# Kernel tuning notes

Hardware: AMD Instinct MI355X
Metric: run time of the kernel (lower is better)

## Reference

```python
import jax, jax.numpy as jnp
import numpy as np

B, S, D = 64, 256, 512          # batch, seq_len_max, num_dim (= in_dim = nclass)
H, DO = 8, 64                   # num_heads, out_dim per head (H*DO == D)
ALPHA = 0.2                     # leaky_relu negative slope
N = B * S                       # nodes
DEG = 32
E = N * DEG + N                 # random edges + self-loops


def setup_inputs() -> dict:
    key = jax.random.key(0)
    k = jax.random.split(key, 7)
    h = jax.random.normal(k[0], (B, S, D), jnp.float32)
    loops = jnp.arange(N, dtype=jnp.int32)
    src = jnp.concatenate([jax.random.randint(k[1], (N * DEG,), 0, N, jnp.int32), loops])
    dst = jnp.concatenate([jax.random.randint(k[2], (N * DEG,), 0, N, jnp.int32), loops])
    W1 = jax.random.normal(k[3], (H, D, DO), jnp.float32) * 0.05      # per-head fc weight
    a1 = jax.random.normal(k[4], (H, 2 * DO), jnp.float32) * 0.05     # per-head attn_fc weight
    Wout = jax.random.normal(k[5], (H * DO, D), jnp.float32) * 0.05   # out_att fc
    aout = jax.random.normal(k[6], (2 * D,), jnp.float32) * 0.05      # out_att attn_fc
    return {"h": h, "W1": W1, "a1": a1, "Wout": Wout, "aout": aout, "src": src, "dst": dst}


def gat_head(x, W, a, src, dst, concat):
    # x: [N, in_d], W: [in_d, d], a: [2d]
    z = x @ W                                   # [N, d]
    d = W.shape[1]
    es = z @ a[:d]                              # src part of attn score, [N]
    ed = z @ a[d:]                              # dst part, [N]
    e = jax.nn.leaky_relu(es[src] + ed[dst], ALPHA)   # [E]
    # segment softmax over incoming edges of each dst node
    m = jax.ops.segment_max(e, dst, num_segments=N)
    m = jnp.where(jnp.isfinite(m), m, 0.0)
    ex = jnp.exp(e - m[dst])
    den = jax.ops.segment_sum(ex, dst, num_segments=N)
    att = ex / den[dst]                         # [E] (self-loops guarantee den > 0)
    out = jax.ops.segment_sum(att[:, None] * z[src], dst, num_segments=N)  # [N, d]
    return jax.nn.elu(out) if concat else out


def reference(h, W1, a1, Wout, aout, src, dst):
    x = h.reshape(N, D)                         # dropout is identity at eval
    heads = jax.vmap(lambda W, a: gat_head(x, W, a, src, dst, True))(W1, a1)  # [H, N, DO]
    hcat = jnp.transpose(heads, (1, 0, 2)).reshape(N, H * DO)                 # [N, H*DO]
    out = jax.nn.elu(gat_head(hcat, Wout, aout, src, dst, False))             # [N, D]
    return (out + x).reshape(B, S, D)
```

## Files before the change

### kernel.cpp

```cpp
#include <hip/hip_runtime.h>
#include <stdint.h>

#define DD 512
#define HH 8
#define DOO 64
#define ALPHA 0.2f

typedef __attribute__((ext_vector_type(8))) short short8;
typedef __attribute__((ext_vector_type(4))) float floatx4;
typedef __attribute__((ext_vector_type(4))) unsigned short u16x4;
typedef unsigned short u16;

static __device__ __forceinline__ float bf2f(u16 u){
  union { unsigned int u; float f; } c; c.u = ((unsigned int)u) << 16; return c.f;
}
static __device__ __forceinline__ u16 f2bf(float f){
  union { float f; unsigned int u; } c; c.f = f;
  unsigned int u = c.u;
  unsigned int r = (u + 0x7FFFu + ((u >> 16) & 1u)) >> 16;
  return (u16)r;
}
static __device__ __forceinline__ float leaky(float s){ return (s >= 0.f) ? s : ALPHA * s; }
static __device__ __forceinline__ float elu(float v){ return (v > 0.f) ? v : (__expf(v) - 1.f); }

#define PERM_LO 0x01000504u
#define PERM_HI 0x03020706u

#define DOT2(accv, pairv, wv) \
  asm("v_dot2_f32_bf16 %0, %1, %2, %0" : "+v"(accv) : "v"(pairv), "v"(wv))

#define DOTS8(ZA, ZB, AQ) do{ unsigned pr_; \
  pr_=__builtin_amdgcn_perm((ZA).x,(ZB).x,PERM_LO); DOT2(acc[0],pr_,(AQ)); \
  pr_=__builtin_amdgcn_perm((ZA).x,(ZB).x,PERM_HI); DOT2(acc[1],pr_,(AQ)); \
  pr_=__builtin_amdgcn_perm((ZA).y,(ZB).y,PERM_LO); DOT2(acc[2],pr_,(AQ)); \
  pr_=__builtin_amdgcn_perm((ZA).y,(ZB).y,PERM_HI); DOT2(acc[3],pr_,(AQ)); \
  pr_=__builtin_amdgcn_perm((ZA).z,(ZB).z,PERM_LO); DOT2(acc[4],pr_,(AQ)); \
  pr_=__builtin_amdgcn_perm((ZA).z,(ZB).z,PERM_HI); DOT2(acc[5],pr_,(AQ)); \
  pr_=__builtin_amdgcn_perm((ZA).w,(ZB).w,PERM_LO); DOT2(acc[6],pr_,(AQ)); \
  pr_=__builtin_amdgcn_perm((ZA).w,(ZB).w,PERM_HI); DOT2(acc[7],pr_,(AQ)); \
}while(0)

#define GLOAD_LDS16(g, l) \
  __builtin_amdgcn_global_load_lds((const __attribute__((address_space(1))) void*)(g), \
                                   (__attribute__((address_space(3))) void*)(l), 16, 0, 0)

static __device__ __forceinline__ uint4 rowl(const u16* __restrict__ zp, int s, int lane){
  return ((const uint4*)(zp + ((size_t)(unsigned)s << 9)))[lane];
}

__global__ void k_prep(const float* __restrict__ h, u16* __restrict__ xb,
                       const float* __restrict__ W1, u16* __restrict__ wbt1,
                       const float* __restrict__ Wout, u16* __restrict__ wbt2,
                       const int* __restrict__ dst, int* deg,
                       int n4, int E){
  int i = blockIdx.x * blockDim.x + threadIdx.x;
  if (i < n4){
    float4 v = ((const float4*)h)[i];
    u16x4 o;
    o[0] = f2bf(v.x); o[1] = f2bf(v.y); o[2] = f2bf(v.z); o[3] = f2bf(v.w);
    ((u16x4*)xb)[i] = o;
    return;
  }
  i -= n4;
  if (i < HH * DD * DOO / 8){
    int idx0 = i * 8;
    #pragma unroll
    for (int t = 0; t < 8; t++){
      int idx = idx0 + t;
      int hh = idx >> 15;
      int rem = idx & 32767;
      int k = rem >> 6;
      int dd = rem & 63;
      wbt1[(hh * 64 + dd) * DD + k] = f2bf(W1[idx]);
    }
    return;
  }
  i -= HH * DD * DOO / 8;
  if (i < DD * DD){
    int k = i >> 9, n = i & 511;
    wbt2[n * DD + k] = f2bf(Wout[i]);
    return;
  }
  i -= DD * DD;
  if (i < E) atomicAdd(&deg[dst[i]], 1);
}

__global__ void k_scan(const int* __restrict__ deg, int* __restrict__ off, int N){
  __shared__ int sm[1024];
  int tid = threadIdx.x;
  const int per = 16;
  int base = tid * per;
  int loc[per];
  int t = 0;
  #pragma unroll
  for (int i = 0; i < per; i++){
    int v = (base + i < N) ? deg[base + i] : 0;
    v = (v + 3) & ~3;
    loc[i] = v; t += v;
  }
  sm[tid] = t; __syncthreads();
  for (int o = 1; o < 1024; o <<= 1){
    int v = 0;
    if (tid >= o) v = sm[tid - o];
    __syncthreads();
    sm[tid] += v;
    __syncthreads();
  }
  int run = sm[tid] - t;
  #pragma unroll
  for (int i = 0; i < per; i++){ if (base + i < N) off[base + i] = run; run += loc[i]; }
  if (tid == 1023) off[N] = run;
}

__global__ void k_scatter(const int* __restrict__ src, const int* __restrict__ dst,
                          const int* __restrict__ off, int* cursor, int* __restrict__ csr,
                          int E, int N){
  int i = blockIdx.x * blockDim.x + threadIdx.x;
  if (i < 256){
    csr[off[N] + i] = 0;
  }
  if (i < E){
    int d = dst[i];
    int p = atomicAdd(&cursor[d], 1);
    csr[off[d] + p] = src[i];
  }
}

__global__ __launch_bounds__(256) void k_gemm(const u16* __restrict__ A,
                                              const u16* __restrict__ BT,
                                              u16* __restrict__ C, int M){
  __shared__ __attribute__((aligned(16))) u16 As[128 * 64];
  __shared__ __attribute__((aligned(16))) u16 Bs[128 * 64];
  const int tid = threadIdx.x;
  const int wid = tid >> 6, lane = tid & 63;
  const int n0 = blockIdx.x * 128, m0 = blockIdx.y * 128;
  const int wr = wid >> 1, wc = wid & 1;
  const int row16 = lane & 15, kg = lane >> 4;
  floatx4 acc[4][4];
  #pragma unroll
  for (int i = 0; i < 4; i++)
    #pragma unroll
    for (int j = 0; j < 4; j++) acc[i][j] = (floatx4)0.0f;

  for (int kt = 0; kt < DD; kt += 64){
    #pragma unroll
    for (int i = 0; i < 4; i++){
      int chunk = i * 256 + tid;
      int m = chunk >> 3, g = chunk & 7;
      int gs = g ^ (m & 7);
      GLOAD_LDS16(A + (size_t)(m0 + m) * DD + kt + gs * 8, &As[chunk * 8]);
      GLOAD_LDS16(BT + (size_t)(n0 + m) * DD + kt + gs * 8, &Bs[chunk * 8]);
    }
    __syncthreads();
    short8 af[4][2], bf[4][2];
    #pragma unroll
    for (int mi = 0; mi < 4; mi++)
      #pragma unroll
      for (int kk = 0; kk < 2; kk++){
        int row = wr * 64 + mi * 16 + row16;
        int gr = (kk * 4 + kg) ^ (row & 7);
        af[mi][kk] = *(const short8*)(&As[(row * 8 + gr) * 8]);
      }
    #pragma unroll
    for (int ni = 0; ni < 4; ni++)
      #pragma unroll
      for (int kk = 0; kk < 2; kk++){
        int row = wc * 64 + ni * 16 + row16;
        int gr = (kk * 4 + kg) ^ (row & 7);
        bf[ni][kk] = *(const short8*)(&Bs[(row * 8 + gr) * 8]);
      }
    #pragma unroll
    for (int kk = 0; kk < 2; kk++)
      #pragma unroll
      for (int mi = 0; mi < 4; mi++)
        #pragma unroll
        for (int ni = 0; ni < 4; ni++)
          acc[mi][ni] = __builtin_amdgcn_mfma_f32_16x16x32_bf16(af[mi][kk], bf[ni][kk], acc[mi][ni], 0, 0, 0);
    __syncthreads();
  }
  #pragma unroll
  for (int mi = 0; mi < 4; mi++)
    #pragma unroll
    for (int ni = 0; ni < 4; ni++)
      #pragma unroll
      for (int j = 0; j < 4; j++){
        int r = m0 + wr * 64 + mi * 16 + kg * 4 + j;
        int c = n0 + wc * 64 + ni * 16 + row16;
        C[(size_t)r * DD + c] = f2bf(acc[mi][ni][j]);
      }
}

__global__ void k_scores1(const u16* __restrict__ z, const float* __restrict__ a1,
                          float* __restrict__ es, float* __restrict__ ed, int N){
  int wid = threadIdx.x >> 6, lane = threadIdx.x & 63;
  int n = blockIdx.x * 4 + wid;
  if (n >= N) return;
  int h = lane >> 3, j8 = lane & 7;
  short8 zv = *(const short8*)(z + (size_t)n * DD + lane * 8);
  float esv = 0.f, edv = 0.f;
  #pragma unroll
  for (int t = 0; t < 8; t++){
    float f = bf2f((u16)zv[t]);
    esv += f * a1[h * 128 + j8 * 8 + t];
    edv += f * a1[h * 128 + 64 + j8 * 8 + t];
  }
  #pragma unroll
  for (int d2 = 1; d2 < 8; d2 <<= 1){ esv += __shfl_xor(esv, d2); edv += __shfl_xor(edv, d2); }
  if (j8 == 0){ es[n * 8 + h] = esv; ed[n * 8 + h] = edv; }
}

__global__ void k_scores2(const u16* __restrict__ z, const float* __restrict__ aout,
                          float* __restrict__ es, float* __restrict__ ed, int N){
  int wid = threadIdx.x >> 6, lane = threadIdx.x & 63;
  int n = blockIdx.x * 4 + wid;
  if (n >= N) return;
  short8 zv = *(const short8*)(z + (size_t)n * DD + lane * 8);
  float esv = 0.f, edv = 0.f;
  #pragma unroll
  for (int t = 0; t < 8; t++){
    float f = bf2f((u16)zv[t]);
    esv += f * aout[lane * 8 + t];
    edv += f * aout[512 + lane * 8 + t];
  }
  #pragma unroll
  for (int d2 = 1; d2 < 64; d2 <<= 1){ esv += __shfl_xor(esv, d2); edv += __shfl_xor(edv, d2); }
  if (lane == 0){ es[n] = esv; ed[n] = edv; }
}

__global__ void k_edgew1(const float* __restrict__ es, const float* __restrict__ ed,
                         const int* __restrict__ off, const int* __restrict__ deg,
                         int* __restrict__ csr, unsigned* __restrict__ wp,
                         float* __restrict__ den1, int N){
  int wid = threadIdx.x >> 6, lane = threadIdx.x & 63;
  int n = blockIdx.x * 4 + wid;
  if (n >= N) return;
  int o0 = off[n], cntp = off[n + 1] - o0, cnt = deg[n];
  float edh[8];
  {
    float4 d0 = *(const float4*)(ed + (size_t)n * 8);
    float4 d1 = *(const float4*)(ed + (size_t)n * 8 + 4);
    edh[0]=d0.x; edh[1]=d0.y; edh[2]=d0.z; edh[3]=d0.w;
    edh[4]=d1.x; edh[5]=d1.y; edh[6]=d1.z; edh[7]=d1.w;
  }
  float den[8];
  #pragma unroll
  for (int h = 0; h < 8; h++) den[h] = 0.f;
  for (int base = 0; base < cntp; base += 64){
    int e = base + lane;
    float wv[8];
    if (e < cnt){
      int s = csr[o0 + e];
      float4 e0 = *(const float4*)(es + (size_t)s * 8);
      float4 e1 = *(const float4*)(es + (size_t)s * 8 + 4);
      float ev[8] = {e0.x, e0.y, e0.z, e0.w, e1.x, e1.y, e1.z, e1.w};
      #pragma unroll
      for (int h = 0; h < 8; h++){
        float w = __expf(leaky(ev[h] + edh[h]));
        wv[h] = w; den[h] += w;
      }
    } else {
      if (e < cntp) csr[o0 + e] = 0;
      #pragma unroll
      for (int h = 0; h < 8; h++) wv[h] = 0.f;
    }
    unsigned pk[8];
    #pragma unroll
    for (int h = 0; h < 8; h++){
      float wn = __shfl_down(wv[h], 1);
      asm("v_cvt_pk_bf16_f32 %0, %1, %2" : "=v"(pk[h]) : "v"(wv[h]), "v"(wn));
    }
    if (!(lane & 1) && e < cntp){
      size_t q = (size_t)((o0 + e) >> 1) * 8;
      uint4 v0; v0.x = pk[0]; v0.y = pk[1]; v0.z = pk[2]; v0.w = pk[3];
      uint4 v1; v1.x = pk[4]; v1.y = pk[5]; v1.z = pk[6]; v1.w = pk[7];
      *(uint4*)(wp + q) = v0;
      *(uint4*)(wp + q + 4) = v1;
    }
  }
  #pragma unroll
  for (int h = 0; h < 8; h++){
    float d = den[h];
    #pragma unroll
    for (int d2 = 1; d2 < 64; d2 <<= 1) d += __shfl_xor(d, d2);
    if (lane == 0) den1[(size_t)n * 8 + h] = d;
  }
}

__global__ void k_edgew2(const float* __restrict__ es, const float* __restrict__ ed,
                         const int* __restrict__ off, const int* __restrict__ deg,
                         int* __restrict__ csr, unsigned* __restrict__ wp,
                         float* __restrict__ den2, int N){
  int wid = threadIdx.x >> 6, lane = threadIdx.x & 63;
  int n = blockIdx.x * 4 + wid;
  if (n >= N) return;
  int o0 = off[n], cntp = off[n + 1] - o0, cnt = deg[n];
  float edn = ed[n];
  float dsum = 0.f;
  for (int base = 0; base < cntp; base += 64){
    int e = base + lane;
    float w = 0.f;
    if (e < cnt){
      int s = csr[o0 + e];
      w = __expf(leaky(es[s] + edn));
      dsum += w;
    } else if (e < cntp){
      csr[o0 + e] = 0;
    }
    float wn = __shfl_down(w, 1);
    if (!(lane & 1) && e < cntp){
      unsigned pk;
      asm("v_cvt_pk_bf16_f32 %0, %1, %2" : "=v"(pk) : "v"(w), "v"(wn));
      wp[(o0 + e) >> 1] = pk;
    }
  }
  #pragma unroll
  for (int d2 = 1; d2 < 64; d2 <<= 1) dsum += __shfl_xor(dsum, d2);
  if (lane == 0) den2[n] = dsum;
}

__global__ __launch_bounds__(256) void k_agg1(const u16* __restrict__ z,
    const unsigned* __restrict__ wp, const float* __restrict__ den1,
    const int* __restrict__ off, const int* __restrict__ csr,
    u16* __restrict__ hcat, int N){
  int wid = __builtin_amdgcn_readfirstlane(threadIdx.x >> 6);
  int lane = threadIdx.x & 63;
  int n = blockIdx.x * 4 + wid;
  if (n >= N) return;
  int o0 = off[n];
  int itn = (off[n + 1] - o0) >> 2;
  const int4* cp4 = (const int4*)(csr + o0);
  int pb = o0 >> 1;
  int head = lane >> 3;
  const unsigned* wpb = wp + (size_t)pb * 8 + head;
  float acc[8];
  #pragma unroll
  for (int j = 0; j < 8; j++) acc[j] = 0.f;

  uint4 zA0, zA1, zB0, zB1;
  unsigned aqA, aqB;
  int4 c1;
  {
    int4 c0 = cp4[0];
    c1 = cp4[1];
    zA0 = rowl(z, c0.x, lane); zA1 = rowl(z, c0.y, lane);
    zB0 = rowl(z, c0.z, lane); zB1 = rowl(z, c0.w, lane);
    aqA = wpb[0]; aqB = wpb[8];
  }
  for (int it = 0; it < itn; ++it){
    int4 cn = cp4[it + 2];
    uint4 nA0 = rowl(z, c1.x, lane), nA1 = rowl(z, c1.y, lane);
    uint4 nB0 = rowl(z, c1.z, lane), nB1 = rowl(z, c1.w, lane);
    unsigned naqA = wpb[(size_t)(2 * it + 2) * 8];
    unsigned naqB = wpb[(size_t)(2 * it + 3) * 8];
    DOTS8(zA0, zA1, aqA);
    DOTS8(zB0, zB1, aqB);
    zA0 = nA0; zA1 = nA1; zB0 = nB0; zB1 = nB1;
    aqA = naqA; aqB = naqB; c1 = cn;
  }
  float inv = 1.f / den1[(size_t)n * 8 + head];
  short8 o;
  #pragma unroll
  for (int j = 0; j < 8; j++) o[j] = (short)f2bf(elu(acc[j] * inv));
  *(short8*)(hcat + (size_t)n * DD + lane * 8) = o;
}

__global__ __launch_bounds__(256) void k_agg2(const u16* __restrict__ z,
    const unsigned* __restrict__ wp, const float* __restrict__ den2,
    const int* __restrict__ off, const int* __restrict__ csr,
    const u16* __restrict__ xb, float* __restrict__ out, int N){
  int wid = __builtin_amdgcn_readfirstlane(threadIdx.x >> 6);
  int lane = threadIdx.x & 63;
  int n = blockIdx.x * 4 + wid;
  if (n >= N) return;
  int o0 = off[n];
  int itn = (off[n + 1] - o0) >> 2;
  const int4* cp4 = (const int4*)(csr + o0);
  int pb = o0 >> 1;
  float acc[8];
  #pragma unroll
  for (int j = 0; j < 8; j++) acc[j] = 0.f;

  uint4 zA0, zA1, zB0, zB1;
  unsigned aqA, aqB;
  int4 c1;
  {
    int4 c0 = cp4[0];
    c1 = cp4[1];
    zA0 = rowl(z, c0.x, lane); zA1 = rowl(z, c0.y, lane);
    zB0 = rowl(z, c0.z, lane); zB1 = rowl(z, c0.w, lane);
    uint2 a01 = *(const uint2*)(wp + pb);
    aqA = a01.x; aqB = a01.y;
  }
  for (int it = 0; it < itn; ++it){
    int4 cn = cp4[it + 2];
    uint4 nA0 = rowl(z, c1.x, lane), nA1 = rowl(z, c1.y, lane);
    uint4 nB0 = rowl(z, c1.z, lane), nB1 = rowl(z, c1.w, lane);
    uint2 an = *(const uint2*)(wp + pb + 2 * it + 2);
    DOTS8(zA0, zA1, aqA);
    DOTS8(zB0, zB1, aqB);
    zA0 = nA0; zA1 = nA1; zB0 = nB0; zB1 = nB1;
    aqA = an.x; aqB = an.y; c1 = cn;
  }
  float inv = 1.f / den2[n];
  short8 xv = *(const short8*)(xb + (size_t)n * DD + lane * 8);
  float ov[8];
  #pragma unroll
  for (int j = 0; j < 8; j++) ov[j] = elu(acc[j] * inv) + bf2f((u16)xv[j]);
  float4 o0v, o1v;
  o0v.x = ov[0]; o0v.y = ov[1]; o0v.z = ov[2]; o0v.w = ov[3];
  o1v.x = ov[4]; o1v.y = ov[5]; o1v.z = ov[6]; o1v.w = ov[7];
  *(float4*)(out + (size_t)n * DD + lane * 8) = o0v;
  *(float4*)(out + (size_t)n * DD + lane * 8 + 4) = o1v;
}

extern "C" void kernel_launch(void* const* d_in, const int* in_sizes, int n_in,
                              void* d_out, int out_size, void* d_ws, size_t ws_size,
                              hipStream_t stream){
  const float* h   = (const float*)d_in[0];
  const float* W1  = (const float*)d_in[1];
  const float* a1  = (const float*)d_in[2];
  const float* Wout= (const float*)d_in[3];
  const float* aout= (const float*)d_in[4];
  const int* src   = (const int*)d_in[5];
  const int* dst   = (const int*)d_in[6];
  float* out = (float*)d_out;
  const int N = in_sizes[0] / DD;
  const int E = in_sizes[5];
  const int EP = E + 3 * N + 512;
  const int ep2 = EP >> 1;

  char* p = (char*)d_ws;
  auto alloc = [&](size_t bytes) -> char* {
    char* r = p;
    p += (bytes + 255) & ~(size_t)255;
    return r;
  };
  u16* xb    = (u16*)alloc((size_t)N * DD * 2);
  u16* z1b   = (u16*)alloc((size_t)N * DD * 2);
  u16* hcat  = (u16*)alloc((size_t)N * DD * 2);
  u16* wbt1  = (u16*)alloc((size_t)DD * DD * 2);
  u16* wbt2  = (u16*)alloc((size_t)DD * DD * 2);
  float* es1 = (float*)alloc((size_t)N * HH * 4);
  float* ed1 = (float*)alloc((size_t)N * HH * 4);
  float* es2 = (float*)alloc((size_t)N * 4);
  float* ed2 = (float*)alloc((size_t)N * 4);
  float* den1= (float*)alloc((size_t)N * HH * 4);
  float* den2= (float*)alloc((size_t)N * 4);
  int* deg   = (int*)alloc((size_t)N * 4);
  int* off   = (int*)alloc((size_t)(N + 1) * 4);
  int* cursor= (int*)alloc((size_t)N * 4);
  int* csr   = (int*)alloc((size_t)EP * 4);
  unsigned* wp1 = (unsigned*)alloc(((size_t)ep2 * 8 + 64) * 4);
  unsigned* wp2 = (unsigned*)alloc(((size_t)ep2 + 64) * 4);

  hipMemsetAsync(deg, 0, (size_t)((char*)csr - (char*)deg), stream);

  int n4 = N * DD / 4;
  int prep_threads = n4 + HH * DD * DOO / 8 + DD * DD + E;
  k_prep<<<(prep_threads + 255) / 256, 256, 0, stream>>>(h, xb, W1, wbt1, Wout, wbt2, dst, deg, n4, E);
  k_scan<<<1, 1024, 0, stream>>>(deg, off, N);
  k_scatter<<<(E + 255) / 256, 256, 0, stream>>>(src, dst, off, cursor, csr, E, N);

  dim3 gg(DD / 128, N / 128);
  dim3 ga((N + 3) / 4);

  k_gemm<<<gg, 256, 0, stream>>>(xb, wbt1, z1b, N);
  k_scores1<<<(N + 3) / 4, 256, 0, stream>>>(z1b, a1, es1, ed1, N);
  k_edgew1<<<ga, 256, 0, stream>>>(es1, ed1, off, deg, csr, wp1, den1, N);
  k_agg1<<<ga, 256, 0, stream>>>(z1b, wp1, den1, off, csr, hcat, N);

  k_gemm<<<gg, 256, 0, stream>>>(hcat, wbt2, z1b, N);
  k_scores2<<<(N + 3) / 4, 256, 0, stream>>>(z1b, aout, es2, ed2, N);
  k_edgew2<<<ga, 256, 0, stream>>>(es2, ed2, off, deg, csr, wp2, den2, N);
  k_agg2<<<ga, 256, 0, stream>>>(z1b, wp2, den2, off, csr, xb, out, N);
}
```

Measured before the change: 281.3 us.

## Split aggregation feature dimension across grid.y and store edge weights head-major

The aggregation kernels now launch four blocks per node group along grid.y. Each wave handles a 128-column slice, so each lane gathers 4 bytes per neighbor row instead of 16, with two accumulators instead of eight. Layer-1 edge weights are stored head-major (one plane per head), so each lane reads a contiguous pair of packed weights for its own head. This raises parallelism and occupancy, with fewer registers per lane. The cost is re-reading the CSR indices four times and issuing many narrower scattered gathers.

```diff
diff --git a/kernel.cpp b/kernel.cpp
--- a/kernel.cpp
+++ b/kernel.cpp
@@ -29,24 +29,9 @@
 #define DOT2(accv, pairv, wv) \
   asm("v_dot2_f32_bf16 %0, %1, %2, %0" : "+v"(accv) : "v"(pairv), "v"(wv))
 
-#define DOTS8(ZA, ZB, AQ) do{ unsigned pr_; \
-  pr_=__builtin_amdgcn_perm((ZA).x,(ZB).x,PERM_LO); DOT2(acc[0],pr_,(AQ)); \
-  pr_=__builtin_amdgcn_perm((ZA).x,(ZB).x,PERM_HI); DOT2(acc[1],pr_,(AQ)); \
-  pr_=__builtin_amdgcn_perm((ZA).y,(ZB).y,PERM_LO); DOT2(acc[2],pr_,(AQ)); \
-  pr_=__builtin_amdgcn_perm((ZA).y,(ZB).y,PERM_HI); DOT2(acc[3],pr_,(AQ)); \
-  pr_=__builtin_amdgcn_perm((ZA).z,(ZB).z,PERM_LO); DOT2(acc[4],pr_,(AQ)); \
-  pr_=__builtin_amdgcn_perm((ZA).z,(ZB).z,PERM_HI); DOT2(acc[5],pr_,(AQ)); \
-  pr_=__builtin_amdgcn_perm((ZA).w,(ZB).w,PERM_LO); DOT2(acc[6],pr_,(AQ)); \
-  pr_=__builtin_amdgcn_perm((ZA).w,(ZB).w,PERM_HI); DOT2(acc[7],pr_,(AQ)); \
-}while(0)
-
 #define GLOAD_LDS16(g, l) \
   __builtin_amdgcn_global_load_lds((const __attribute__((address_space(1))) void*)(g), \
                                    (__attribute__((address_space(3))) void*)(l), 16, 0, 0)
-
-static __device__ __forceinline__ uint4 rowl(const u16* __restrict__ zp, int s, int lane){
-  return ((const uint4*)(zp + ((size_t)(unsigned)s << 9)))[lane];
-}
 
 __global__ void k_prep(const float* __restrict__ h, u16* __restrict__ xb,
                        const float* __restrict__ W1, u16* __restrict__ wbt1,
@@ -230,7 +215,7 @@
 __global__ void k_edgew1(const float* __restrict__ es, const float* __restrict__ ed,
                          const int* __restrict__ off, const int* __restrict__ deg,
                          int* __restrict__ csr, unsigned* __restrict__ wp,
-                         float* __restrict__ den1, int N){
+                         float* __restrict__ den1, int N, int ep2){
   int wid = threadIdx.x >> 6, lane = threadIdx.x & 63;
   int n = blockIdx.x * 4 + wid;
   if (n >= N) return;
@@ -263,18 +248,14 @@
       #pragma unroll
       for (int h = 0; h < 8; h++) wv[h] = 0.f;
     }
-    unsigned pk[8];
     #pragma unroll
     for (int h = 0; h < 8; h++){
       float wn = __shfl_down(wv[h], 1);
-      asm("v_cvt_pk_bf16_f32 %0, %1, %2" : "=v"(pk[h]) : "v"(wv[h]), "v"(wn));
-    }
-    if (!(lane & 1) && e < cntp){
-      size_t q = (size_t)((o0 + e) >> 1) * 8;
-      uint4 v0; v0.x = pk[0]; v0.y = pk[1]; v0.z = pk[2]; v0.w = pk[3];
-      uint4 v1; v1.x = pk[4]; v1.y = pk[5]; v1.z = pk[6]; v1.w = pk[7];
-      *(uint4*)(wp + q) = v0;
-      *(uint4*)(wp + q + 4) = v1;
+      if (!(lane & 1) && e < cntp){
+        unsigned pk;
+        asm("v_cvt_pk_bf16_f32 %0, %1, %2" : "=v"(pk) : "v"(wv[h]), "v"(wn));
+        wp[(size_t)h * ep2 + ((o0 + e) >> 1)] = pk;
+      }
     }
   }
   #pragma unroll
@@ -321,47 +302,44 @@
 __global__ __launch_bounds__(256) void k_agg1(const u16* __restrict__ z,
     const unsigned* __restrict__ wp, const float* __restrict__ den1,
     const int* __restrict__ off, const int* __restrict__ csr,
-    u16* __restrict__ hcat, int N){
+    u16* __restrict__ hcat, int N, int ep2){
   int wid = __builtin_amdgcn_readfirstlane(threadIdx.x >> 6);
   int lane = threadIdx.x & 63;
   int n = blockIdx.x * 4 + wid;
   if (n >= N) return;
+  int p = blockIdx.y;
   int o0 = off[n];
   int itn = (off[n + 1] - o0) >> 2;
   const int4* cp4 = (const int4*)(csr + o0);
-  int pb = o0 >> 1;
-  int head = lane >> 3;
-  const unsigned* wpb = wp + (size_t)pb * 8 + head;
-  float acc[8];
-  #pragma unroll
-  for (int j = 0; j < 8; j++) acc[j] = 0.f;
-
-  uint4 zA0, zA1, zB0, zB1;
-  unsigned aqA, aqB;
-  int4 c1;
-  {
-    int4 c0 = cp4[0];
-    c1 = cp4[1];
-    zA0 = rowl(z, c0.x, lane); zA1 = rowl(z, c0.y, lane);
-    zB0 = rowl(z, c0.z, lane); zB1 = rowl(z, c0.w, lane);
-    aqA = wpb[0]; aqB = wpb[8];
-  }
+  const unsigned* zd = (const unsigned*)z + (size_t)p * 64 + lane;
+  int head = 2 * p + (lane >> 5);
+  const unsigned* wpb = wp + (size_t)head * ep2 + (o0 >> 1);
+  float acc0 = 0.f, acc1 = 0.f;
+
+  int4 c0 = cp4[0], c1 = cp4[1];
+  uint2 a0 = *(const uint2*)(wpb);
+  uint2 a1 = *(const uint2*)(wpb + 2);
+  unsigned dA0 = zd[(size_t)(unsigned)c0.x * 256], dA1 = zd[(size_t)(unsigned)c0.y * 256];
+  unsigned dB0 = zd[(size_t)(unsigned)c0.z * 256], dB1 = zd[(size_t)(unsigned)c0.w * 256];
+  unsigned eA0 = zd[(size_t)(unsigned)c1.x * 256], eA1 = zd[(size_t)(unsigned)c1.y * 256];
+  unsigned eB0 = zd[(size_t)(unsigned)c1.z * 256], eB1 = zd[(size_t)(unsigned)c1.w * 256];
+
   for (int it = 0; it < itn; ++it){
     int4 cn = cp4[it + 2];
-    uint4 nA0 = rowl(z, c1.x, lane), nA1 = rowl(z, c1.y, lane);
-    uint4 nB0 = rowl(z, c1.z, lane), nB1 = rowl(z, c1.w, lane);
-    unsigned naqA = wpb[(size_t)(2 * it + 2) * 8];
-    unsigned naqB = wpb[(size_t)(2 * it + 3) * 8];
-    DOTS8(zA0, zA1, aqA);
-    DOTS8(zB0, zB1, aqB);
-    zA0 = nA0; zA1 = nA1; zB0 = nB0; zB1 = nB1;
-    aqA = naqA; aqB = naqB; c1 = cn;
+    uint2 an = *(const uint2*)(wpb + 2 * it + 4);
+    unsigned nA0 = zd[(size_t)(unsigned)cn.x * 256], nA1 = zd[(size_t)(unsigned)cn.y * 256];
+    unsigned nB0 = zd[(size_t)(unsigned)cn.z * 256], nB1 = zd[(size_t)(unsigned)cn.w * 256];
+    unsigned pr;
+    pr = __builtin_amdgcn_perm(dA0, dA1, PERM_LO); DOT2(acc0, pr, a0.x);
+    pr = __builtin_amdgcn_perm(dA0, dA1, PERM_HI); DOT2(acc1, pr, a0.x);
+    pr = __builtin_amdgcn_perm(dB0, dB1, PERM_LO); DOT2(acc0, pr, a0.y);
+    pr = __builtin_amdgcn_perm(dB0, dB1, PERM_HI); DOT2(acc1, pr, a0.y);
+    dA0 = eA0; dA1 = eA1; dB0 = eB0; dB1 = eB1; a0 = a1;
+    eA0 = nA0; eA1 = nA1; eB0 = nB0; eB1 = nB1; a1 = an;
   }
   float inv = 1.f / den1[(size_t)n * 8 + head];
-  short8 o;
-  #pragma unroll
-  for (int j = 0; j < 8; j++) o[j] = (short)f2bf(elu(acc[j] * inv));
-  *(short8*)(hcat + (size_t)n * DD + lane * 8) = o;
+  unsigned od = (unsigned)f2bf(elu(acc0 * inv)) | ((unsigned)f2bf(elu(acc1 * inv)) << 16);
+  ((unsigned*)(hcat + (size_t)n * DD))[p * 64 + lane] = od;
 }
 
 __global__ __launch_bounds__(256) void k_agg2(const u16* __restrict__ z,
@@ -372,45 +350,41 @@
   int lane = threadIdx.x & 63;
   int n = blockIdx.x * 4 + wid;
   if (n >= N) return;
+  int p = blockIdx.y;
   int o0 = off[n];
   int itn = (off[n + 1] - o0) >> 2;
   const int4* cp4 = (const int4*)(csr + o0);
-  int pb = o0 >> 1;
-  float acc[8];
-  #pragma unroll
-  for (int j = 0; j < 8; j++) acc[j] = 0.f;
-
-  uint4 zA0, zA1, zB0, zB1;
-  unsigned aqA, aqB;
-  int4 c1;
-  {
-    int4 c0 = cp4[0];
-    c1 = cp4[1];
-    zA0 = rowl(z, c0.x, lane); zA1 = rowl(z, c0.y, lane);
-    zB0 = rowl(z, c0.z, lane); zB1 = rowl(z, c0.w, lane);
-    uint2 a01 = *(const uint2*)(wp + pb);
-    aqA = a01.x; aqB = a01.y;
-  }
+  const unsigned* zd = (const unsigned*)z + (size_t)p * 64 + lane;
+  const unsigned* wpb = wp + (o0 >> 1);
+  float acc0 = 0.f, acc1 = 0.f;
+
+  int4 c0 = cp4[0], c1 = cp4[1];
+  uint2 a0 = *(const uint2*)(wpb);
+  uint2 a1 = *(const uint2*)(wpb + 2);
+  unsigned dA0 = zd[(size_t)(unsigned)c0.x * 256], dA1 = zd[(size_t)(unsigned)c0.y * 256];
+  unsigned dB0 = zd[(size_t)(unsigned)c0.z * 256], dB1 = zd[(size_t)(unsigned)c0.w * 256];
+  unsigned eA0 = zd[(size_t)(unsigned)c1.x * 256], eA1 = zd[(size_t)(unsigned)c1.y * 256];
+  unsigned eB0 = zd[(size_t)(unsigned)c1.z * 256], eB1 = zd[(size_t)(unsigned)c1.w * 256];
+
   for (int it = 0; it < itn; ++it){
     int4 cn = cp4[it + 2];
-    uint4 nA0 = rowl(z, c1.x, lane), nA1 = rowl(z, c1.y, lane);
-    uint4 nB0 = rowl(z, c1.z, lane), nB1 = rowl(z, c1.w, lane);
-    uint2 an = *(const uint2*)(wp + pb + 2 * it + 2);
-    DOTS8(zA0, zA1, aqA);
-    DOTS8(zB0, zB1, aqB);
-    zA0 = nA0; zA1 = nA1; zB0 = nB0; zB1 = nB1;
-    aqA = an.x; aqB = an.y; c1 = cn;
+    uint2 an = *(const uint2*)(wpb + 2 * it + 4);
+    unsigned nA0 = zd[(size_t)(unsigned)cn.x * 256], nA1 = zd[(size_t)(unsigned)cn.y * 256];
+    unsigned nB0 = zd[(size_t)(unsigned)cn.z * 256], nB1 = zd[(size_t)(unsigned)cn.w * 256];
+    unsigned pr;
+    pr = __builtin_amdgcn_perm(dA0, dA1, PERM_LO); DOT2(acc0, pr, a0.x);
+    pr = __builtin_amdgcn_perm(dA0, dA1, PERM_HI); DOT2(acc1, pr, a0.x);
+    pr = __builtin_amdgcn_perm(dB0, dB1, PERM_LO); DOT2(acc0, pr, a0.y);
+    pr = __builtin_amdgcn_perm(dB0, dB1, PERM_HI); DOT2(acc1, pr, a0.y);
+    dA0 = eA0; dA1 = eA1; dB0 = eB0; dB1 = eB1; a0 = a1;
+    eA0 = nA0; eA1 = nA1; eB0 = nB0; eB1 = nB1; a1 = an;
   }
   float inv = 1.f / den2[n];
-  short8 xv = *(const short8*)(xb + (size_t)n * DD + lane * 8);
-  float ov[8];
-  #pragma unroll
-  for (int j = 0; j < 8; j++) ov[j] = elu(acc[j] * inv) + bf2f((u16)xv[j]);
-  float4 o0v, o1v;
-  o0v.x = ov[0]; o0v.y = ov[1]; o0v.z = ov[2]; o0v.w = ov[3];
-  o1v.x = ov[4]; o1v.y = ov[5]; o1v.z = ov[6]; o1v.w = ov[7];
-  *(float4*)(out + (size_t)n * DD + lane * 8) = o0v;
-  *(float4*)(out + (size_t)n * DD + lane * 8 + 4) = o1v;
+  unsigned xv = ((const unsigned*)(xb + (size_t)n * DD))[p * 64 + lane];
+  float2 o2;
+  o2.x = elu(acc0 * inv) + bf2f((u16)(xv & 0xFFFFu));
+  o2.y = elu(acc1 * inv) + bf2f((u16)(xv >> 16));
+  *(float2*)(out + (size_t)n * DD + p * 128 + lane * 2) = o2;
 }
 
 extern "C" void kernel_launch(void* const* d_in, const int* in_sizes, int n_in,
@@ -450,7 +424,7 @@
   int* off   = (int*)alloc((size_t)(N + 1) * 4);
   int* cursor= (int*)alloc((size_t)N * 4);
   int* csr   = (int*)alloc((size_t)EP * 4);
-  unsigned* wp1 = (unsigned*)alloc(((size_t)ep2 * 8 + 64) * 4);
+  unsigned* wp1 = (unsigned*)alloc(((size_t)HH * ep2 + 64) * 4);
   unsigned* wp2 = (unsigned*)alloc(((size_t)ep2 + 64) * 4);
 
   hipMemsetAsync(deg, 0, (size_t)((char*)csr - (char*)deg), stream);
@@ -462,15 +436,16 @@
   k_scatter<<<(E + 255) / 256, 256, 0, stream>>>(src, dst, off, cursor, csr, E, N);
 
   dim3 gg(DD / 128, N / 128);
-  dim3 ga((N + 3) / 4);
+  dim3 ga((N + 3) / 4, 4);
+  dim3 gw((N + 3) / 4);
 
   k_gemm<<<gg, 256, 0, stream>>>(xb, wbt1, z1b, N);
   k_scores1<<<(N + 3) / 4, 256, 0, stream>>>(z1b, a1, es1, ed1, N);
-  k_edgew1<<<ga, 256, 0, stream>>>(es1, ed1, off, deg, csr, wp1, den1, N);
-  k_agg1<<<ga, 256, 0, stream>>>(z1b, wp1, den1, off, csr, hcat, N);
+  k_edgew1<<<gw, 256, 0, stream>>>(es1, ed1, off, deg, csr, wp1, den1, N, ep2);
+  k_agg1<<<ga, 256, 0, stream>>>(z1b, wp1, den1, off, csr, hcat, N, ep2);
 
   k_gemm<<<gg, 256, 0, stream>>>(hcat, wbt2, z1b, N);
   k_scores2<<<(N + 3) / 4, 256, 0, stream>>>(z1b, aout, es2, ed2, N);
-  k_edgew2<<<ga, 256, 0, stream>>>(es2, ed2, off, deg, csr, wp2, den2, N);
+  k_edgew2<<<gw, 256, 0, stream>>>(es2, ed2, off, deg, csr, wp2, den2, N);
   k_agg2<<<ga, 256, 0, stream>>>(z1b, wp2, den2, off, csr, xb, out, N);
 }
```

Result: faster. 252.3 us (-10.3%).

## Bucket CSR neighbor lists by source range for better gather locality

Applied to the files above, without the earlier changes.

The CSR build now counts and scatters edges into 8 sub-buckets per destination node, keyed by the high bits of the source index. Each bucket is padded to even length with a sentinel node N whose z row is zeroed. The edge-weight kernels treat that sentinel as zero weight instead of rewriting csr. The intent is to make the neighbor gathers in the aggregation kernels more cache-local by ordering sources within each row. The cost is more padding, an extra fill kernel, larger degree, offset and cursor arrays, and the readfirstlane hint on wave id is dropped.

```diff
diff --git a/kernel.cpp b/kernel.cpp
--- a/kernel.cpp
+++ b/kernel.cpp
@@ -51,8 +51,9 @@
 __global__ void k_prep(const float* __restrict__ h, u16* __restrict__ xb,
                        const float* __restrict__ W1, u16* __restrict__ wbt1,
                        const float* __restrict__ Wout, u16* __restrict__ wbt2,
-                       const int* __restrict__ dst, int* deg,
-                       int n4, int E){
+                       const int* __restrict__ src, const int* __restrict__ dst,
+                       int* deg8, u16* __restrict__ z1b,
+                       int n4, int E, int N, int bshift){
   int i = blockIdx.x * blockDim.x + threadIdx.x;
   if (i < n4){
     float4 v = ((const float4*)h)[i];
@@ -82,10 +83,19 @@
     return;
   }
   i -= DD * DD;
-  if (i < E) atomicAdd(&deg[dst[i]], 1);
-}
-
-__global__ void k_scan(const int* __restrict__ deg, int* __restrict__ off, int N){
+  if (i < E){
+    atomicAdd(&deg8[(size_t)dst[i] * 8 + (src[i] >> bshift)], 1);
+    return;
+  }
+  i -= E;
+  if (i < DD / 4){
+    u16x4 zz; zz[0]=0; zz[1]=0; zz[2]=0; zz[3]=0;
+    ((u16x4*)(z1b + (size_t)N * DD))[i] = zz;
+  }
+}
+
+__global__ void k_scan(const int* __restrict__ deg8, int* __restrict__ bop,
+                       int* __restrict__ cursor8, int* __restrict__ off, int N){
   __shared__ int sm[1024];
   int tid = threadIdx.x;
   const int per = 16;
@@ -94,9 +104,25 @@
   int t = 0;
   #pragma unroll
   for (int i = 0; i < per; i++){
-    int v = (base + i < N) ? deg[base + i] : 0;
-    v = (v + 3) & ~3;
-    loc[i] = v; t += v;
+    int n = base + i;
+    int s = 0;
+    if (n < N){
+      int4 d0 = ((const int4*)deg8)[(size_t)n * 2];
+      int4 d1 = ((const int4*)deg8)[(size_t)n * 2 + 1];
+      int4 p0, p1;
+      p0.x = s; s += (d0.x + 1) & ~1;
+      p0.y = s; s += (d0.y + 1) & ~1;
+      p0.z = s; s += (d0.z + 1) & ~1;
+      p0.w = s; s += (d0.w + 1) & ~1;
+      p1.x = s; s += (d1.x + 1) & ~1;
+      p1.y = s; s += (d1.y + 1) & ~1;
+      p1.z = s; s += (d1.z + 1) & ~1;
+      p1.w = s; s += (d1.w + 1) & ~1;
+      if (s & 2) s += 2;
+      ((int4*)bop)[(size_t)n * 2] = p0;
+      ((int4*)bop)[(size_t)n * 2 + 1] = p1;
+    }
+    loc[i] = s; t += s;
   }
   sm[tid] = t; __syncthreads();
   for (int o = 1; o < 1024; o <<= 1){
@@ -108,22 +134,44 @@
   }
   int run = sm[tid] - t;
   #pragma unroll
-  for (int i = 0; i < per; i++){ if (base + i < N) off[base + i] = run; run += loc[i]; }
+  for (int i = 0; i < per; i++){
+    int n = base + i;
+    if (n < N){
+      off[n] = run;
+      int4 b0 = ((const int4*)bop)[(size_t)n * 2];
+      int4 b1 = ((const int4*)bop)[(size_t)n * 2 + 1];
+      int4 c0, c1;
+      c0.x = run + b0.x; c0.y = run + b0.y; c0.z = run + b0.z; c0.w = run + b0.w;
+      c1.x = run + b1.x; c1.y = run + b1.y; c1.z = run + b1.z; c1.w = run + b1.w;
+      ((int4*)cursor8)[(size_t)n * 2] = c0;
+      ((int4*)cursor8)[(size_t)n * 2 + 1] = c1;
+      run += loc[i];
+    }
+  }
   if (tid == 1023) off[N] = run;
 }
 
 __global__ void k_scatter(const int* __restrict__ src, const int* __restrict__ dst,
-                          const int* __restrict__ off, int* cursor, int* __restrict__ csr,
-                          int E, int N){
+                          const int* __restrict__ off, int* cursor8, int* __restrict__ csr,
+                          int E, int N, int bshift){
   int i = blockIdx.x * blockDim.x + threadIdx.x;
-  if (i < 256){
-    csr[off[N] + i] = 0;
+  if (i < 512){
+    csr[off[N] + i] = N;
   }
   if (i < E){
-    int d = dst[i];
-    int p = atomicAdd(&cursor[d], 1);
-    csr[off[d] + p] = src[i];
-  }
+    int d = dst[i], s = src[i];
+    int p = atomicAdd(&cursor8[(size_t)d * 8 + (s >> bshift)], 1);
+    csr[p] = s;
+  }
+}
+
+__global__ void k_fillpad(const int* __restrict__ off, const int* __restrict__ bop,
+                          const int* __restrict__ cursor8, int* __restrict__ csr, int N){
+  int t = blockIdx.x * blockDim.x + threadIdx.x;
+  if (t >= N * 8) return;
+  int n = t >> 3, b = t & 7;
+  int segend = (b == 7) ? off[n + 1] : off[n] + bop[n * 8 + b + 1];
+  for (int q = cursor8[t]; q < segend; q++) csr[q] = N;
 }
 
 __global__ __launch_bounds__(256) void k_gemm(const u16* __restrict__ A,
@@ -228,13 +276,13 @@
 }
 
 __global__ void k_edgew1(const float* __restrict__ es, const float* __restrict__ ed,
-                         const int* __restrict__ off, const int* __restrict__ deg,
-                         int* __restrict__ csr, unsigned* __restrict__ wp,
+                         const int* __restrict__ off,
+                         const int* __restrict__ csr, unsigned* __restrict__ wp,
                          float* __restrict__ den1, int N){
   int wid = threadIdx.x >> 6, lane = threadIdx.x & 63;
   int n = blockIdx.x * 4 + wid;
   if (n >= N) return;
-  int o0 = off[n], cntp = off[n + 1] - o0, cnt = deg[n];
+  int o0 = off[n], cntp = off[n + 1] - o0;
   float edh[8];
   {
     float4 d0 = *(const float4*)(ed + (size_t)n * 8);
@@ -247,21 +295,17 @@
   for (int h = 0; h < 8; h++) den[h] = 0.f;
   for (int base = 0; base < cntp; base += 64){
     int e = base + lane;
+    int s = csr[o0 + e];
+    bool valid = (e < cntp) && (s != N);
+    float4 e0 = *(const float4*)(es + (size_t)s * 8);
+    float4 e1 = *(const float4*)(es + (size_t)s * 8 + 4);
+    float ev[8] = {e0.x, e0.y, e0.z, e0.w, e1.x, e1.y, e1.z, e1.w};
     float wv[8];
-    if (e < cnt){
-      int s = csr[o0 + e];
-      float4 e0 = *(const float4*)(es + (size_t)s * 8);
-      float4 e1 = *(const float4*)(es + (size_t)s * 8 + 4);
-      float ev[8] = {e0.x, e0.y, e0.z, e0.w, e1.x, e1.y, e1.z, e1.w};
-      #pragma unroll
-      for (int h = 0; h < 8; h++){
-        float w = __expf(leaky(ev[h] + edh[h]));
-        wv[h] = w; den[h] += w;
-      }
-    } else {
-      if (e < cntp) csr[o0 + e] = 0;
-      #pragma unroll
-      for (int h = 0; h < 8; h++) wv[h] = 0.f;
+    #pragma unroll
+    for (int h = 0; h < 8; h++){
+      float w = __expf(leaky(ev[h] + edh[h]));
+      wv[h] = valid ? w : 0.f;
+      den[h] += wv[h];
     }
     unsigned pk[8];
     #pragma unroll
@@ -287,25 +331,22 @@
 }
 
 __global__ void k_edgew2(const float* __restrict__ es, const float* __restrict__ ed,
-                         const int* __restrict__ off, const int* __restrict__ deg,
-                         int* __restrict__ csr, unsigned* __restrict__ wp,
+                         const int* __restrict__ off,
+                         const int* __restrict__ csr, unsigned* __restrict__ wp,
                          float* __restrict__ den2, int N){
   int wid = threadIdx.x >> 6, lane = threadIdx.x & 63;
   int n = blockIdx.x * 4 + wid;
   if (n >= N) return;
-  int o0 = off[n], cntp = off[n + 1] - o0, cnt = deg[n];
+  int o0 = off[n], cntp = off[n + 1] - o0;
   float edn = ed[n];
   float dsum = 0.f;
   for (int base = 0; base < cntp; base += 64){
     int e = base + lane;
-    float w = 0.f;
-    if (e < cnt){
-      int s = csr[o0 + e];
-      w = __expf(leaky(es[s] + edn));
-      dsum += w;
-    } else if (e < cntp){
-      csr[o0 + e] = 0;
-    }
+    int s = csr[o0 + e];
+    bool valid = (e < cntp) && (s != N);
+    float w = __expf(leaky(es[s] + edn));
+    w = valid ? w : 0.f;
+    dsum += w;
     float wn = __shfl_down(w, 1);
     if (!(lane & 1) && e < cntp){
       unsigned pk;
@@ -322,7 +363,7 @@
     const unsigned* __restrict__ wp, const float* __restrict__ den1,
     const int* __restrict__ off, const int* __restrict__ csr,
     u16* __restrict__ hcat, int N){
-  int wid = __builtin_amdgcn_readfirstlane(threadIdx.x >> 6);
+  int wid = threadIdx.x >> 6;
   int lane = threadIdx.x & 63;
   int n = blockIdx.x * 4 + wid;
   if (n >= N) return;
@@ -368,7 +409,7 @@
     const unsigned* __restrict__ wp, const float* __restrict__ den2,
     const int* __restrict__ off, const int* __restrict__ csr,
     const u16* __restrict__ xb, float* __restrict__ out, int N){
-  int wid = __builtin_amdgcn_readfirstlane(threadIdx.x >> 6);
+  int wid = threadIdx.x >> 6;
   int lane = threadIdx.x & 63;
   int n = blockIdx.x * 4 + wid;
   if (n >= N) return;
@@ -426,7 +467,9 @@
   float* out = (float*)d_out;
   const int N = in_sizes[0] / DD;
   const int E = in_sizes[5];
-  const int EP = E + 3 * N + 512;
+  int bshift = 0;
+  while ((8 << bshift) < N) bshift++;
+  const int EP = E + 10 * N + 512;
   const int ep2 = EP >> 1;
 
   char* p = (char*)d_ws;
@@ -436,41 +479,44 @@
     return r;
   };
   u16* xb    = (u16*)alloc((size_t)N * DD * 2);
-  u16* z1b   = (u16*)alloc((size_t)N * DD * 2);
+  u16* z1b   = (u16*)alloc((size_t)(N + 1) * DD * 2);
   u16* hcat  = (u16*)alloc((size_t)N * DD * 2);
   u16* wbt1  = (u16*)alloc((size_t)DD * DD * 2);
   u16* wbt2  = (u16*)alloc((size_t)DD * DD * 2);
-  float* es1 = (float*)alloc((size_t)N * HH * 4);
+  float* es1 = (float*)alloc(((size_t)N * HH + 8) * 4);
   float* ed1 = (float*)alloc((size_t)N * HH * 4);
-  float* es2 = (float*)alloc((size_t)N * 4);
+  float* es2 = (float*)alloc(((size_t)N + 8) * 4);
   float* ed2 = (float*)alloc((size_t)N * 4);
   float* den1= (float*)alloc((size_t)N * HH * 4);
   float* den2= (float*)alloc((size_t)N * 4);
-  int* deg   = (int*)alloc((size_t)N * 4);
+  int* deg8  = (int*)alloc((size_t)N * 8 * 4);
+  int* bop   = (int*)alloc((size_t)N * 8 * 4);
+  int* cursor8 = (int*)alloc((size_t)N * 8 * 4);
   int* off   = (int*)alloc((size_t)(N + 1) * 4);
-  int* cursor= (int*)alloc((size_t)N * 4);
   int* csr   = (int*)alloc((size_t)EP * 4);
   unsigned* wp1 = (unsigned*)alloc(((size_t)ep2 * 8 + 64) * 4);
   unsigned* wp2 = (unsigned*)alloc(((size_t)ep2 + 64) * 4);
 
-  hipMemsetAsync(deg, 0, (size_t)((char*)csr - (char*)deg), stream);
+  hipMemsetAsync(deg8, 0, (size_t)N * 8 * 4, stream);
 
   int n4 = N * DD / 4;
-  int prep_threads = n4 + HH * DD * DOO / 8 + DD * DD + E;
-  k_prep<<<(prep_threads + 255) / 256, 256, 0, stream>>>(h, xb, W1, wbt1, Wout, wbt2, dst, deg, n4, E);
-  k_scan<<<1, 1024, 0, stream>>>(deg, off, N);
-  k_scatter<<<(E + 255) / 256, 256, 0, stream>>>(src, dst, off, cursor, csr, E, N);
+  int prep_threads = n4 + HH * DD * DOO / 8 + DD * DD + E + DD / 4;
+  k_prep<<<(prep_threads + 255) / 256, 256, 0, stream>>>(h, xb, W1, wbt1, Wout, wbt2,
+                                                         src, dst, deg8, z1b, n4, E, N, bshift);
+  k_scan<<<1, 1024, 0, stream>>>(deg8, bop, cursor8, off, N);
+  k_scatter<<<(E + 255) / 256, 256, 0, stream>>>(src, dst, off, cursor8, csr, E, N, bshift);
+  k_fillpad<<<(N * 8 + 255) / 256, 256, 0, stream>>>(off, bop, cursor8, csr, N);
 
   dim3 gg(DD / 128, N / 128);
   dim3 ga((N + 3) / 4);
 
   k_gemm<<<gg, 256, 0, stream>>>(xb, wbt1, z1b, N);
   k_scores1<<<(N + 3) / 4, 256, 0, stream>>>(z1b, a1, es1, ed1, N);
-  k_edgew1<<<ga, 256, 0, stream>>>(es1, ed1, off, deg, csr, wp1, den1, N);
+  k_edgew1<<<ga, 256, 0, stream>>>(es1, ed1, off, csr, wp1, den1, N);
   k_agg1<<<ga, 256, 0, stream>>>(z1b, wp1, den1, off, csr, hcat, N);
 
   k_gemm<<<gg, 256, 0, stream>>>(hcat, wbt2, z1b, N);
   k_scores2<<<(N + 3) / 4, 256, 0, stream>>>(z1b, aout, es2, ed2, N);
-  k_edgew2<<<ga, 256, 0, stream>>>(es2, ed2, off, deg, csr, wp2, den2, N);
+  k_edgew2<<<ga, 256, 0, stream>>>(es2, ed2, off, csr, wp2, den2, N);
   k_agg2<<<ga, 256, 0, stream>>>(z1b, wp2, den2, off, csr, xb, out, N);
 }
```

Result: slower. 348.9 us (+24.0%).
